# Kernel tuning notes

Measured on AMD Instinct MI355X. Metric: run time of the kernel, lower is better.

## Reference

```python
import jax, jax.numpy as jnp
import numpy as np

B, T, E, H = 8, 2048, 1024, 64

def setup_inputs() -> dict:
    key = jax.random.key(0)
    k1, k2, k3, k4 = jax.random.split(key, 4)
    x = jax.random.normal(k1, (B, T, E), dtype=jnp.float32)
    # Linear(E, H, bias=False) weights stored as [E, H] (x @ W)
    s = 1.0 / np.sqrt(E)
    Wk = jax.random.normal(k2, (E, H), dtype=jnp.float32) * s
    Wq = jax.random.normal(k3, (E, H), dtype=jnp.float32) * s
    Wv = jax.random.normal(k4, (E, H), dtype=jnp.float32) * s
    return {"x": x, "Wk": Wk, "Wq": Wq, "Wv": Wv}

def reference(x, Wk, Wq, Wv):
    _, t, e = x.shape
    k = jnp.einsum('bte,eh->bth', x, Wk)
    q = jnp.einsum('bte,eh->bth', x, Wq)
    v = jnp.einsum('bte,eh->bth', x, Wv)
    # NOTE: original scales by E**-0.5 (embedding dim), not head_size**-0.5
    wei = jnp.einsum('bqh,bkh->bqk', q, k) * (e ** -0.5)
    causal = jnp.tril(jnp.ones((t, t), dtype=bool))
    wei = jnp.where(causal, wei, -jnp.inf)
    wei = jax.nn.softmax(wei, axis=-1)
    out = jnp.einsum('bqk,bkh->bqh', wei, v)
    return out
```

## Files before the change

### kernel.cpp

```cpp
#include <hip/hip_runtime.h>

typedef unsigned short u16;
typedef unsigned int u32;
typedef __bf16 bf16x8 __attribute__((ext_vector_type(8)));
typedef __bf16 bf16x4 __attribute__((ext_vector_type(4)));
typedef float f32x4 __attribute__((ext_vector_type(4)));

constexpr int Bn = 8, Tn = 2048, En = 1024, Hn = 64;
constexpr int Mrows = Bn * Tn;
constexpr float CEXP = 0.03125f * 1.4426950408889634f;

__device__ __forceinline__ u16 f2bf(float f) {
  u32 u = __float_as_uint(f);
  return (u16)((u + 0x7fffu + ((u >> 16) & 1u)) >> 16);
}

__global__ __launch_bounds__(256) void wt_kernel(
    const float* __restrict__ Wk, const float* __restrict__ Wq,
    const float* __restrict__ Wv, u16* __restrict__ Wt) {
  __shared__ u16 tile[64][72];
  const int mat = blockIdx.x >> 4;
  const int k0 = (blockIdx.x & 15) * 64;
  const float* W = (mat == 0) ? Wk : (mat == 1) ? Wq : Wv;
  const int t = threadIdx.x;
  {
    const int kl = t >> 2;
    const int h0 = (t & 3) * 16;
    const float4* src = (const float4*)(W + (size_t)(k0 + kl) * Hn + h0);
#pragma unroll
    for (int i = 0; i < 4; ++i) {
      float4 v = src[i];
      tile[h0 + 4 * i + 0][kl] = f2bf(v.x);
      tile[h0 + 4 * i + 1][kl] = f2bf(v.y);
      tile[h0 + 4 * i + 2][kl] = f2bf(v.z);
      tile[h0 + 4 * i + 3][kl] = f2bf(v.w);
    }
  }
  __syncthreads();
  {
    const int hl = t >> 2;
    const int kk = (t & 3) * 16;
    uint4 a = *(const uint4*)&tile[hl][kk];
    uint4 b = *(const uint4*)&tile[hl][kk + 8];
    u16* dst = Wt + (size_t)mat * Hn * En + (size_t)hl * En + k0 + kk;
    *(uint4*)dst = a;
    *(uint4*)(dst + 8) = b;
  }
}

__global__ __launch_bounds__(256, 2) void qkv_kernel(
    const float* __restrict__ x, const u16* __restrict__ Wt,
    u16* __restrict__ Kb16, u16* __restrict__ Qb16, u16* __restrict__ Vt16) {
  constexpr int NR = 32, BK = 64, LDK = BK + 8;
  __shared__ u16 xs[NR * LDK];
  const int t = threadIdx.x;
  const int w = t >> 6, lane = t & 63;
  const int quad = lane >> 4, l16 = lane & 15;
  const int r0 = blockIdx.x * NR;

  const int srow = t >> 3, schunk = t & 7;
  const float* xp = x + (size_t)(r0 + srow) * En + schunk * 8;
  u16* xsw = xs + srow * LDK + schunk * 8;

  const u16* wpb = Wt + (size_t)l16 * En + quad * 8;

  f32x4 acc[3][2];
#pragma unroll
  for (int i = 0; i < 3; ++i)
#pragma unroll
    for (int nt = 0; nt < 2; ++nt) acc[i][nt] = (f32x4){0.f, 0.f, 0.f, 0.f};

  float4 pre0 = *(const float4*)(xp);
  float4 pre1 = *(const float4*)(xp + 4);

  for (int k0 = 0; k0 < En; k0 += BK) {
    __syncthreads();
    {
      bf16x8 pk;
      pk[0] = (__bf16)pre0.x; pk[1] = (__bf16)pre0.y;
      pk[2] = (__bf16)pre0.z; pk[3] = (__bf16)pre0.w;
      pk[4] = (__bf16)pre1.x; pk[5] = (__bf16)pre1.y;
      pk[6] = (__bf16)pre1.z; pk[7] = (__bf16)pre1.w;
      *(bf16x8*)xsw = pk;
    }
    __syncthreads();
    if (k0 + BK < En) {
      pre0 = *(const float4*)(xp + k0 + BK);
      pre1 = *(const float4*)(xp + k0 + BK + 4);
    }
#pragma unroll
    for (int ks = 0; ks < 2; ++ks) {
      bf16x8 b0 = *(const bf16x8*)(xs + l16 * LDK + ks * 32 + quad * 8);
      bf16x8 b1 = *(const bf16x8*)(xs + (16 + l16) * LDK + ks * 32 + quad * 8);
#pragma unroll
      for (int i = 0; i < 3; ++i) {
        const int mt = 3 * w + i;
        bf16x8 a = *(const bf16x8*)(wpb + (size_t)(mt * 16) * En + k0 + ks * 32);
        acc[i][0] = __builtin_amdgcn_mfma_f32_16x16x32_bf16(a, b0, acc[i][0], 0, 0, 0);
        acc[i][1] = __builtin_amdgcn_mfma_f32_16x16x32_bf16(a, b1, acc[i][1], 0, 0, 0);
      }
    }
  }

#pragma unroll
  for (int i = 0; i < 3; ++i) {
    const int mt = 3 * w + i;
    const int mat = mt >> 2, ht = mt & 3;
#pragma unroll
    for (int nt = 0; nt < 2; ++nt) {
      const int row = r0 + nt * 16 + l16;
      f32x4 a = acc[i][nt];
      if (mat < 2) {
        u16* dst = ((mat == 0) ? Kb16 : Qb16) + (size_t)row * Hn + ht * 16 + quad * 4;
        uint2 pk;
        pk.x = (u32)f2bf(a[0]) | ((u32)f2bf(a[1]) << 16);
        pk.y = (u32)f2bf(a[2]) | ((u32)f2bf(a[3]) << 16);
        *(uint2*)dst = pk;
      } else {
        const int bb = row >> 11, tt = row & 2047;
        u16* base = Vt16 + ((size_t)bb * 64) * Tn + tt;
#pragma unroll
        for (int r = 0; r < 4; ++r)
          base[(size_t)(ht * 16 + quad * 4 + r) * Tn] = f2bf(a[r]);
      }
    }
  }
}

__global__ __launch_bounds__(256, 4) void attn_kernel(
    const u16* __restrict__ Qb16, const u16* __restrict__ Kb16,
    const u16* __restrict__ Vt16, float* __restrict__ out) {
  __shared__ u16 pt[2][4][16][40];
  __shared__ float l_sh[4][16];
  __shared__ float o_sh[4][16][68];

  const int idx = blockIdx.x;
  const int b = idx & 7;
  const int tq = 127 - (idx >> 3);
  const int w = threadIdx.x >> 6, lane = threadIdx.x & 63;
  const int quad = lane >> 4, l16 = lane & 15;
  const int qbase = tq * 16;
  const int limit = qbase + 16;
  const int ch = ((limit + 127) >> 7) << 5;
  const int lo = w * ch;
  const int hi = min(lo + ch, limit);
  const int q_abs = qbase + l16;

  const u16* Kp = Kb16 + (size_t)b * Tn * Hn;
  const u16* Vp = Vt16 + (size_t)b * 64 * Tn;

  const u16* qrow = Qb16 + ((size_t)b * Tn + q_abs) * Hn + quad * 8;
  const bf16x8 qb0 = *(const bf16x8*)(qrow);
  const bf16x8 qb1 = *(const bf16x8*)(qrow + 32);

  f32x4 od0 = {0.f, 0.f, 0.f, 0.f}, od1 = od0, od2 = od0, od3 = od0;
  f32x4 lacc = {0.f, 0.f, 0.f, 0.f};

#pragma unroll 2
  for (int kb = lo; kb < hi; kb += 32) {
    const int par = (kb >> 5) & 1;
    const u16* krow0 = Kp + (size_t)(kb + l16) * Hn + quad * 8;
    const u16* krow1 = krow0 + (size_t)16 * Hn;
    f32x4 z = {0.f, 0.f, 0.f, 0.f};
    f32x4 st0 = __builtin_amdgcn_mfma_f32_16x16x32_bf16(*(const bf16x8*)(krow0), qb0, z, 0, 0, 0);
    st0 = __builtin_amdgcn_mfma_f32_16x16x32_bf16(*(const bf16x8*)(krow0 + 32), qb1, st0, 0, 0, 0);
    f32x4 st1 = __builtin_amdgcn_mfma_f32_16x16x32_bf16(*(const bf16x8*)(krow1), qb0, z, 0, 0, 0);
    st1 = __builtin_amdgcn_mfma_f32_16x16x32_bf16(*(const bf16x8*)(krow1 + 32), qb1, st1, 0, 0, 0);

    if (kb + 15 > qbase) {
#pragma unroll
      for (int r = 0; r < 4; ++r)
        if (kb + quad * 4 + r > q_abs) st0[r] = -3.0e38f;
    }
    if (kb + 31 > qbase) {
#pragma unroll
      for (int r = 0; r < 4; ++r)
        if (kb + 16 + quad * 4 + r > q_abs) st1[r] = -3.0e38f;
    }

    f32x4 p0, p1;
#pragma unroll
    for (int r = 0; r < 4; ++r) {
      p0[r] = __builtin_amdgcn_exp2f(st0[r] * CEXP);
      p1[r] = __builtin_amdgcn_exp2f(st1[r] * CEXP);
    }
    lacc += p0;
    lacc += p1;

    {
      bf16x4 w0, w1;
      w0[0] = (__bf16)p0[0]; w0[1] = (__bf16)p0[1];
      w0[2] = (__bf16)p0[2]; w0[3] = (__bf16)p0[3];
      w1[0] = (__bf16)p1[0]; w1[1] = (__bf16)p1[1];
      w1[2] = (__bf16)p1[2]; w1[3] = (__bf16)p1[3];
      *(bf16x4*)&pt[par][w][l16][quad * 4] = w0;
      *(bf16x4*)&pt[par][w][l16][16 + quad * 4] = w1;
    }
    const bf16x8 pb = *(const bf16x8*)&pt[par][w][l16][quad * 8];

    const u16* vrow = Vp + (size_t)l16 * Tn + kb + quad * 8;
    od0 = __builtin_amdgcn_mfma_f32_16x16x32_bf16(*(const bf16x8*)(vrow), pb, od0, 0, 0, 0);
    od1 = __builtin_amdgcn_mfma_f32_16x16x32_bf16(*(const bf16x8*)(vrow + (size_t)16 * Tn), pb, od1, 0, 0, 0);
    od2 = __builtin_amdgcn_mfma_f32_16x16x32_bf16(*(const bf16x8*)(vrow + (size_t)32 * Tn), pb, od2, 0, 0, 0);
    od3 = __builtin_amdgcn_mfma_f32_16x16x32_bf16(*(const bf16x8*)(vrow + (size_t)48 * Tn), pb, od3, 0, 0, 0);
  }

  float l = (lacc[0] + lacc[1]) + (lacc[2] + lacc[3]);
  l += __shfl_xor(l, 16);
  l += __shfl_xor(l, 32);
  if (quad == 0) l_sh[w][l16] = l;
  *(f32x4*)&o_sh[w][l16][0 * 16 + quad * 4] = od0;
  *(f32x4*)&o_sh[w][l16][1 * 16 + quad * 4] = od1;
  *(f32x4*)&o_sh[w][l16][2 * 16 + quad * 4] = od2;
  *(f32x4*)&o_sh[w][l16][3 * 16 + quad * 4] = od3;
  __syncthreads();

  const int qq = threadIdx.x >> 4, dq = threadIdx.x & 15;
  float lg = 0.f;
  f32x4 acc = {0.f, 0.f, 0.f, 0.f};
#pragma unroll
  for (int ww = 0; ww < 4; ++ww) {
    lg += l_sh[ww][qq];
    acc += *(const f32x4*)&o_sh[ww][qq][dq * 4];
  }
  acc *= (1.f / lg);
  *(f32x4*)(out + ((size_t)b * Tn + qbase + qq) * Hn + dq * 4) = acc;
}

extern "C" void kernel_launch(void* const* d_in, const int* in_sizes, int n_in,
                              void* d_out, int out_size, void* d_ws, size_t ws_size,
                              hipStream_t stream) {
  const void* x = nullptr;
  const void* Ws[3] = {nullptr, nullptr, nullptr};
  int wj = 0;
  for (int i = 0; i < n_in; ++i) {
    if (in_sizes[i] == Bn * Tn * En) x = d_in[i];
    else if (wj < 3) Ws[wj++] = d_in[i];
  }
  const float* Wk = (const float*)Ws[0];
  const float* Wq = (const float*)Ws[1];
  const float* Wv = (const float*)Ws[2];

  u16* Kb16 = (u16*)d_ws;
  u16* Qb16 = Kb16 + (size_t)Mrows * Hn;
  u16* Vt16 = Qb16 + (size_t)Mrows * Hn;
  u16* Wt   = Vt16 + (size_t)Mrows * Hn;

  wt_kernel<<<48, 256, 0, stream>>>(Wk, Wq, Wv, Wt);
  qkv_kernel<<<Mrows / 32, 256, 0, stream>>>((const float*)x, Wt, Kb16, Qb16, Vt16);
  attn_kernel<<<Bn * (Tn / 16), 256, 0, stream>>>(Qb16, Kb16, Vt16, (float*)d_out);
}
```

Before: 158.4 us.

## Pipeline QKV projection with async global-to-LDS loads and triple buffering

The QKV projection kernel now stages fp32 x tiles straight into LDS with global_load_lds instead of going through registers. It triple-buffers them with XOR-swizzled addresses and converts to bf16 at fragment-read time. Weight fragments are double-buffered in registers, and hand-placed vmcnt waits plus barriers overlap loads with MFMA work. The aim is to hide global load latency and remove the register round trip and the extra sync per k-step. In exchange the LDS footprint grows (fp32, three buffers), and correctness now depends on the hand-counted vmcnt values.

```diff
diff --git a/kernel.cpp b/kernel.cpp
--- a/kernel.cpp
+++ b/kernel.cpp
@@ -13,6 +13,12 @@
 __device__ __forceinline__ u16 f2bf(float f) {
   u32 u = __float_as_uint(f);
   return (u16)((u + 0x7fffu + ((u >> 16) & 1u)) >> 16);
+}
+
+__device__ __forceinline__ void gload16(const void* g, void* l) {
+  __builtin_amdgcn_global_load_lds(
+      (const __attribute__((address_space(1))) void*)g,
+      (__attribute__((address_space(3))) void*)l, 16, 0, 0);
 }
 
 __global__ __launch_bounds__(256) void wt_kernel(
@@ -51,56 +57,118 @@
 __global__ __launch_bounds__(256, 2) void qkv_kernel(
     const float* __restrict__ x, const u16* __restrict__ Wt,
     u16* __restrict__ Kb16, u16* __restrict__ Qb16, u16* __restrict__ Vt16) {
-  constexpr int NR = 32, BK = 64, LDK = BK + 8;
-  __shared__ u16 xs[NR * LDK];
+  constexpr int BK = 64;
+  __shared__ __align__(16) float xs[3][32 * BK];
   const int t = threadIdx.x;
   const int w = t >> 6, lane = t & 63;
   const int quad = lane >> 4, l16 = lane & 15;
-  const int r0 = blockIdx.x * NR;
-
-  const int srow = t >> 3, schunk = t & 7;
-  const float* xp = x + (size_t)(r0 + srow) * En + schunk * 8;
-  u16* xsw = xs + srow * LDK + schunk * 8;
+  const int r0 = blockIdx.x * 32;
+
+  const int rj0 = w * 8 + (lane >> 4);
+  const int rj1 = rj0 + 4;
+  const float* gsrc0 = x + (size_t)(r0 + rj0) * En + (((lane & 15) ^ (rj0 & 15)) << 2);
+  const float* gsrc1 = x + (size_t)(r0 + rj1) * En + (((lane & 15) ^ (rj1 & 15)) << 2);
 
   const u16* wpb = Wt + (size_t)l16 * En + quad * 8;
 
+  int ofs[2][2];
+#pragma unroll
+  for (int ks = 0; ks < 2; ++ks) {
+    ofs[ks][0] = ((ks * 8 + quad * 2) ^ l16) << 2;
+    ofs[ks][1] = ((ks * 8 + quad * 2 + 1) ^ l16) << 2;
+  }
+
   f32x4 acc[3][2];
 #pragma unroll
   for (int i = 0; i < 3; ++i)
 #pragma unroll
     for (int nt = 0; nt < 2; ++nt) acc[i][nt] = (f32x4){0.f, 0.f, 0.f, 0.f};
 
-  float4 pre0 = *(const float4*)(xp);
-  float4 pre1 = *(const float4*)(xp + 4);
-
-  for (int k0 = 0; k0 < En; k0 += BK) {
-    __syncthreads();
-    {
-      bf16x8 pk;
-      pk[0] = (__bf16)pre0.x; pk[1] = (__bf16)pre0.y;
-      pk[2] = (__bf16)pre0.z; pk[3] = (__bf16)pre0.w;
-      pk[4] = (__bf16)pre1.x; pk[5] = (__bf16)pre1.y;
-      pk[6] = (__bf16)pre1.z; pk[7] = (__bf16)pre1.w;
-      *(bf16x8*)xsw = pk;
-    }
-    __syncthreads();
-    if (k0 + BK < En) {
-      pre0 = *(const float4*)(xp + k0 + BK);
-      pre1 = *(const float4*)(xp + k0 + BK + 4);
-    }
-#pragma unroll
-    for (int ks = 0; ks < 2; ++ks) {
-      bf16x8 b0 = *(const bf16x8*)(xs + l16 * LDK + ks * 32 + quad * 8);
-      bf16x8 b1 = *(const bf16x8*)(xs + (16 + l16) * LDK + ks * 32 + quad * 8);
-#pragma unroll
-      for (int i = 0; i < 3; ++i) {
-        const int mt = 3 * w + i;
-        bf16x8 a = *(const bf16x8*)(wpb + (size_t)(mt * 16) * En + k0 + ks * 32);
-        acc[i][0] = __builtin_amdgcn_mfma_f32_16x16x32_bf16(a, b0, acc[i][0], 0, 0, 0);
-        acc[i][1] = __builtin_amdgcn_mfma_f32_16x16x32_bf16(a, b1, acc[i][1], 0, 0, 0);
-      }
-    }
-  }
+  bf16x8 afA[3][2], afB[3][2];
+
+#define STAGE(P, K0)                              \
+  do {                                            \
+    gload16(gsrc0 + (K0), (P) + w * 512);         \
+    gload16(gsrc1 + (K0), (P) + w * 512 + 256);   \
+  } while (0)
+
+#define LOADA(DST, K0)                                                              \
+  do {                                                                              \
+    _Pragma("unroll") for (int i_ = 0; i_ < 3; ++i_)                                \
+        _Pragma("unroll") for (int ks_ = 0; ks_ < 2; ++ks_)                         \
+            DST[i_][ks_] = *(const bf16x8*)(wpb + (size_t)((3 * w + i_) * 16) * En + \
+                                            (K0) + ks_ * 32);                       \
+  } while (0)
+
+#define CVT8(LO, HI, R)                                       \
+  do {                                                        \
+    R[0] = (__bf16)LO[0]; R[1] = (__bf16)LO[1];               \
+    R[2] = (__bf16)LO[2]; R[3] = (__bf16)LO[3];               \
+    R[4] = (__bf16)HI[0]; R[5] = (__bf16)HI[1];               \
+    R[6] = (__bf16)HI[2]; R[7] = (__bf16)HI[3];               \
+  } while (0)
+
+#define COMPUTE(P, AF)                                                             \
+  do {                                                                             \
+    const float* xa_ = (P) + l16 * 64;                                             \
+    const float* xb_ = (P) + (l16 + 16) * 64;                                      \
+    _Pragma("unroll") for (int ks_ = 0; ks_ < 2; ++ks_) {                          \
+      f32x4 lo0_ = *(const f32x4*)(xa_ + ofs[ks_][0]);                             \
+      f32x4 hi0_ = *(const f32x4*)(xa_ + ofs[ks_][1]);                             \
+      f32x4 lo1_ = *(const f32x4*)(xb_ + ofs[ks_][0]);                             \
+      f32x4 hi1_ = *(const f32x4*)(xb_ + ofs[ks_][1]);                             \
+      bf16x8 b0_, b1_;                                                             \
+      CVT8(lo0_, hi0_, b0_);                                                       \
+      CVT8(lo1_, hi1_, b1_);                                                       \
+      _Pragma("unroll") for (int i_ = 0; i_ < 3; ++i_) {                           \
+        acc[i_][0] = __builtin_amdgcn_mfma_f32_16x16x32_bf16(AF[i_][ks_], b0_,     \
+                                                             acc[i_][0], 0, 0, 0); \
+        acc[i_][1] = __builtin_amdgcn_mfma_f32_16x16x32_bf16(AF[i_][ks_], b1_,     \
+                                                             acc[i_][1], 0, 0, 0); \
+      }                                                                            \
+    }                                                                              \
+  } while (0)
+
+#define WAITBAR(N)                                          \
+  do {                                                      \
+    asm volatile("s_waitcnt vmcnt(" #N ")" ::: "memory");   \
+    __builtin_amdgcn_s_barrier();                           \
+    asm volatile("" ::: "memory");                          \
+  } while (0)
+
+  float* p0 = &xs[0][0];
+  float* p1 = &xs[1][0];
+  float* p2 = &xs[2][0];
+
+  STAGE(p0, 0);
+  STAGE(p1, BK);
+  LOADA(afA, 0);
+
+  for (int tt = 0; tt < 16; tt += 2) {
+    WAITBAR(8);
+    LOADA(afB, (tt + 1) * 64);
+    asm volatile("" ::: "memory");
+    if (tt + 2 < 16) STAGE(p2, (tt + 2) * 64);
+    COMPUTE(p0, afA);
+
+    if (tt == 14) {
+      WAITBAR(6);
+    } else {
+      WAITBAR(8);
+    }
+    if (tt + 2 < 16) LOADA(afA, (tt + 2) * 64);
+    asm volatile("" ::: "memory");
+    if (tt + 3 < 16) STAGE(p0, (tt + 3) * 64);
+    COMPUTE(p1, afB);
+
+    float* tmp = p0; p0 = p2; p2 = p1; p1 = tmp;
+  }
+
+#undef STAGE
+#undef LOADA
+#undef CVT8
+#undef COMPUTE
+#undef WAITBAR
 
 #pragma unroll
   for (int i = 0; i < 3; ++i) {
```

After: 155.2 us. -2.1%, faster.
